# Kernel tuning notes

Hardware: AMD Instinct MI355X
Metric: run time of the kernel (lower is better)

## Reference

```python
import jax, jax.numpy as jnp
import numpy as np
import math

B, C, L, D = 64, 21, 8192, 512
KG, KP = 25, 15  # gaussian decomp kernel, phase-corrector kernel (both odd)
PI = math.pi


def _reflect_pad(x, k):
    # x: [B, C, T]; torch 'same' reflect padding: left = k//2, right = k-1-k//2
    pl = k // 2
    return jnp.pad(x, ((0, 0), (0, 0), (pl, k - 1 - pl)), mode='reflect')


def _depthwise_conv1d(x, w):
    # x: [B, C, T_pad], w: [C, 1, k]  (cross-correlation, groups=C, VALID)
    return jax.lax.conv_general_dilated(
        x, w, window_strides=(1,), padding='VALID',
        dimension_numbers=('NCH', 'OIH', 'NCH'),
        feature_group_count=x.shape[1])


def _phase_unwrap(phase):
    # phase: [B, L, C]; unwrap along time axis=1 (matches torch implementation)
    d = jnp.diff(phase, axis=1)
    d_mod = jnp.mod(d + PI, 2.0 * PI) - PI
    d_mod = jnp.where((d_mod == -PI) & (d > 0), PI, d_mod)
    correction = jnp.cumsum(d_mod - d, axis=1)
    return jnp.concatenate([phase[:, :1, :], phase[:, 1:, :] + correction], axis=1)


def _analytic_signal(x):
    # scipy.signal.hilbert along axis=1; x: [B, L, C], L even
    n = x.shape[1]
    h = np.zeros(n, dtype=np.float32)
    h[0] = 1.0
    h[n // 2] = 1.0
    h[1:n // 2] = 2.0
    Xf = jnp.fft.fft(x, axis=1)
    return jnp.fft.ifft(Xf * jnp.asarray(h)[None, :, None], axis=1)


def setup_inputs() -> dict:
    key = jax.random.key(0)
    ks = jax.random.split(key, 4)
    return {
        'x_input': jax.random.normal(ks[0], (B, C, L), jnp.float32),
        'x_w': jax.random.normal(ks[1], (L, D), jnp.float32) / np.sqrt(L).astype(np.float32),
        'x_b': jnp.zeros((D,), jnp.float32),
        'i_w': jax.random.normal(ks[2], (L, D), jnp.float32) / np.sqrt(L).astype(np.float32),
        'i_b': jnp.zeros((D,), jnp.float32),
        'log_sigma': jnp.full((C,), math.log(3.0), jnp.float32),
        'pc_weight': jax.random.normal(ks[3], (C, 1, KP), jnp.float32) * 0.01,
        'pc_strength': jnp.asarray(0.2, jnp.float32),
        'alpha_log': jnp.zeros((C,), jnp.float32),
        'phi0': jnp.zeros((C,), jnp.float32),
        'beta1_log': jnp.asarray(0.0, jnp.float32),
        'beta2_log': jnp.asarray(0.0, jnp.float32),
    }


def reference(x_input, x_w, x_b, i_w, i_b, log_sigma, pc_weight, pc_strength,
              alpha_log, phi0, beta1_log, beta2_log):
    # x_input: [B, C, L]
    x_out = jax.nn.gelu(x_input @ x_w + x_b, approximate=False)  # [B, C, D]

    # --- decomp_Gaussian (depthwise gaussian low-pass) ---
    half = KG // 2
    idx = jnp.arange(-half, half + 1, dtype=x_input.dtype)
    sigma = jnp.exp(log_sigma)[:, None, None] + 1e-6            # [C,1,1]
    g = jnp.exp(-(idx[None, None, :] ** 2) / (2.0 * sigma * sigma))
    g = g / (g.sum(axis=-1, keepdims=True) + 1e-12)             # [C,1,KG]
    trend_ch = _depthwise_conv1d(_reflect_pad(x_input, KG), g)  # [B,C,L]
    seasonal = (x_input - trend_ch).transpose(0, 2, 1)          # [B,L,C]
    trend = trend_ch.transpose(0, 2, 1)                         # [B,L,C]

    # --- TSCoupler ---
    # hilbert_transform uses .detach() in the original -> stop_gradient
    z = _analytic_signal(jax.lax.stop_gradient(seasonal))
    phase = jnp.arctan2(z.imag, z.real)                         # [B,L,C]
    phase_u = _phase_unwrap(phase)

    # ZeroMeanPhaseCorrector
    w = pc_weight - pc_weight.mean(axis=-1, keepdims=True)
    delta = _depthwise_conv1d(_reflect_pad(phase_u.transpose(0, 2, 1), KP), w)
    phi_corr = phase_u + jnp.tanh(pc_strength) * delta.transpose(0, 2, 1)
    phi_corr = phi_corr + phi0[None, None, :]

    T_clamped = jnp.clip(trend, -10.0, 10.0)
    beta1 = jax.nn.softplus(beta1_log) + 1e-6
    beta2 = jax.nn.softplus(beta2_log) + 1e-6
    A_raw = beta1 * jnp.log1p(jnp.exp(beta2 * T_clamped))       # [B,L,C]
    alpha = jax.nn.softplus(alpha_log)[None, None, :] + 1e-6    # [1,1,C]
    A_t = alpha * A_raw[0]                                      # [1,L,C]  (batch-0 indexing, as in source)
    I = (A_t * jnp.cos(phi_corr)).transpose(0, 2, 1)            # [B,C,L]

    I_coupled = jax.nn.gelu(I @ i_w + i_b, approximate=False)   # [B,C,D]
    return (x_out, I_coupled)
```

## Files before the change

### kernel.cpp

```cpp
#include <hip/hip_runtime.h>
#include <hip/hip_bf16.h>
#include <math.h>

#define LMAX 8192
#define KGAUSS 25

#define PI_F 3.14159265358979323846f
#define TWO_PI_F 6.28318530717958647692f

typedef __hip_bfloat16 bf16;
typedef unsigned short u16;
typedef short bf16x8 __attribute__((ext_vector_type(8)));
typedef float f32x4 __attribute__((ext_vector_type(4)));

__device__ __forceinline__ float b2f(bf16 v) { return __bfloat162float(v); }
__device__ __forceinline__ bf16 f2b(float v) { return __float2bfloat16(v); }
__device__ __forceinline__ float rdv(const void* p, long i, int isb) {
  return isb ? b2f(((const bf16*)p)[i]) : ((const float*)p)[i];
}

__device__ __forceinline__ void async16(const void* g, void* l) {
#if __has_builtin(__builtin_amdgcn_global_load_lds)
  __builtin_amdgcn_global_load_lds((const __attribute__((address_space(1))) void*)g,
                                   (__attribute__((address_space(3))) void*)l, 16, 0, 0);
#else
  *(uint4*)l = *(const uint4*)g;
#endif
}

__device__ __forceinline__ float2 f2add(float2 a, float2 b) {
  return make_float2(a.x + b.x, a.y + b.y);
}
__device__ __forceinline__ float2 f2sub(float2 a, float2 b) {
  return make_float2(a.x - b.x, a.y - b.y);
}
__device__ __forceinline__ float2 cmulc(float2 x, float2 w) {
  return make_float2(x.x * w.x + x.y * w.y, x.y * w.x - x.x * w.y);
}
__device__ __forceinline__ float2 cmul(float2 x, float2 w) {
  return make_float2(x.x * w.x - x.y * w.y, x.x * w.y + x.y * w.x);
}
#define ZI(i) ((i) ^ (((i) >> 4) & 15))

__global__ void k_params(const void* xb, const void* ib, const void* ls, const void* pw,
                         const void* al, const void* ph, const void* ps, const void* b1,
                         const void* b2, float* pf, int* flag, float2* tw,
                         int D, int C, int KP, int L) {
  unsigned wls = ((const unsigned*)ls)[0];
  int isb = ((wls >> 16) == (wls & 0xffffu)) ? 1 : 0;
  int blk = blockIdx.x, t = threadIdx.x;
  if (blk < 64) {
    int i = blk * 256 + t;
    if (i == 0) flag[0] = isb;
    float v = 0.0f;
    if (i < D)                              v = rdv(xb, i, isb);
    else if (i >= 2048 && i < 2048 + D)     v = rdv(ib, i - 2048, isb);
    else if (i >= 4096 && i < 4096 + C)     v = rdv(ls, i - 4096, isb);
    else if (i >= 4352 && i < 4352 + C*KP)  v = rdv(pw, i - 4352, isb);
    else if (i >= 8448 && i < 8448 + C)     v = rdv(al, i - 8448, isb);
    else if (i >= 8704 && i < 8704 + C)     v = rdv(ph, i - 8704, isb);
    else if (i == 8960)                     v = rdv(ps, 0, isb);
    else if (i == 8961)                     v = rdv(b1, 0, isb);
    else if (i == 8962)                     v = rdv(b2, 0, isb);
    pf[i] = v;
  } else {
    int j = (blk - 64) * 256 + t;
    if (j < L / 2) {
      double a = 6.283185307179586476925286766559 * (double)j / (double)L;
      tw[j] = make_float2((float)cos(a), (float)sin(a));
    }
  }
}

__global__ __launch_bounds__(256) void k_transpose(const void* __restrict__ in,
    bf16* __restrict__ out, const int* __restrict__ flag, int K, int N) {
  __shared__ u16 tile[64][65];
  int isb = *flag;
  int r0 = blockIdx.x * 64, c0 = blockIdx.y * 64;
  int t = threadIdx.x;
#pragma unroll
  for (int i = 0; i < 16; ++i) {
    int idx = t + i * 256;
    int r = idx >> 6, cc = idx & 63;
    int gr = r0 + r; gr = gr < K ? gr : K - 1;
    int gc = c0 + cc; gc = gc < N ? gc : N - 1;
    size_t gi = (size_t)gr * N + gc;
    u16 v;
    if (isb) v = ((const u16*)in)[gi];
    else { bf16 h = f2b(((const float*)in)[gi]); v = *(u16*)&h; }
    tile[r][cc] = v;
  }
  __syncthreads();
#pragma unroll
  for (int i = 0; i < 16; ++i) {
    int idx = t + i * 256;
    int a = idx >> 6, bb = idx & 63;
    if (c0 + a < N && r0 + bb < K)
      ((u16*)out)[(size_t)(c0 + a) * K + (r0 + bb)] = tile[bb][a];
  }
}

__global__ __launch_bounds__(256) void k_decomp(const void* __restrict__ x,
    const int* __restrict__ flag, const float* __restrict__ pf,
    float* __restrict__ seasonal, float* __restrict__ trend0,
    bf16* __restrict__ Xb, int C, int L) {
  __shared__ float xs[LMAX];
  int bc = blockIdx.x;
  int c = bc % C, b = bc / C;
  int t = threadIdx.x;
  int isb = *flag;
  for (int i = t; i < L; i += 256) {
    float xv = rdv(x, (size_t)bc * L + i, isb);
    xs[i] = xv;
    Xb[(size_t)bc * L + i] = f2b(xv);
  }
  float sigma = expf(pf[4096 + c]) + 1e-6f;
  float inv2s2 = 1.0f / (2.0f * sigma * sigma);
  float g[KGAUSS];
  float gs = 0.0f;
  for (int j = 0; j < KGAUSS; ++j) {
    float d = (float)(j - 12);
    float v = expf(-(d * d) * inv2s2);
    g[j] = v; gs += v;
  }
  float ginv = 1.0f / (gs + 1e-12f);
  for (int j = 0; j < KGAUSS; ++j) g[j] *= ginv;
  __syncthreads();
  for (int i = t; i < L; i += 256) {
    float acc = 0.0f;
#pragma unroll
    for (int j = 0; j < KGAUSS; ++j) {
      int idx = i + j - 12;
      idx = idx < 0 ? -idx : (idx >= L ? 2 * L - 2 - idx : idx);
      acc += g[j] * xs[idx];
    }
    seasonal[(size_t)bc * L + i] = xs[i] - acc;
    if (b == 0) trend0[(size_t)c * L + i] = acc;
  }
}

__global__ void k_amp(float* __restrict__ trend0, const float* __restrict__ pf,
                      int L) {
  int i = blockIdx.x * 256 + threadIdx.x;
  int c = blockIdx.y;
  if (i >= L) return;
  float alpha = log1pf(expf(pf[8448 + c])) + 1e-6f;
  float beta1 = log1pf(expf(pf[8961])) + 1e-6f;
  float beta2 = log1pf(expf(pf[8962])) + 1e-6f;
  size_t idx = (size_t)c * L + i;
  float T = trend0[idx];
  T = fminf(10.0f, fmaxf(-10.0f, T));
  trend0[idx] = alpha * (beta1 * log1pf(expf(beta2 * T)));
}

__global__ __launch_bounds__(512, 4) void k_hilbert8(float* __restrict__ sp,
    const float2* __restrict__ tw, int L, int lg, long M) {
  __shared__ float2 z[LMAX];
  long r0 = 2L * blockIdx.x;
  int has1 = (r0 + 1 < M) ? 1 : 0;
  float* row0 = sp + (size_t)r0 * L;
  float* row1 = row0 + (has1 ? (size_t)L : 0);
  const int t = threadIdx.x;
  const int T = 512;
  const int nq = L >> 3;

  for (int s = lg; s >= 4; s -= 3) {
    const int h4 = 1 << (s - 3);
    for (int q = t; q < nq; q += T) {
      int pos = q & (h4 - 1);
      int base = ((q >> (s - 3)) << s) + pos;
      float2 E0, E1, E2, E3, E4, E5, E6, E7;
      if (s == lg) {
        int i;
        i = base;          E0 = make_float2(row0[i], has1 ? row1[i] : 0.0f);
        i = base + h4;     E1 = make_float2(row0[i], has1 ? row1[i] : 0.0f);
        i = base + 2*h4;   E2 = make_float2(row0[i], has1 ? row1[i] : 0.0f);
        i = base + 3*h4;   E3 = make_float2(row0[i], has1 ? row1[i] : 0.0f);
        i = base + 4*h4;   E4 = make_float2(row0[i], has1 ? row1[i] : 0.0f);
        i = base + 5*h4;   E5 = make_float2(row0[i], has1 ? row1[i] : 0.0f);
        i = base + 6*h4;   E6 = make_float2(row0[i], has1 ? row1[i] : 0.0f);
        i = base + 7*h4;   E7 = make_float2(row0[i], has1 ? row1[i] : 0.0f);
      } else {
        E0 = z[ZI(base)];          E1 = z[ZI(base + h4)];
        E2 = z[ZI(base + 2*h4)];   E3 = z[ZI(base + 3*h4)];
        E4 = z[ZI(base + 4*h4)];   E5 = z[ZI(base + 5*h4)];
        E6 = z[ZI(base + 6*h4)];   E7 = z[ZI(base + 7*h4)];
      }
      float2 wa0 = tw[pos << (lg - s)];
      float2 wa1 = tw[(pos + h4) << (lg - s)];
      float2 wa2 = tw[(pos + 2*h4) << (lg - s)];
      float2 wa3 = tw[(pos + 3*h4) << (lg - s)];
      float2 wb0 = tw[pos << (lg - s + 1)];
      float2 wb1 = tw[(pos + h4) << (lg - s + 1)];
      float2 wc0 = tw[pos << (lg - s + 2)];
      float2 A0 = f2add(E0, E4), B0 = cmulc(f2sub(E0, E4), wa0);
      float2 A1 = f2add(E1, E5), B1 = cmulc(f2sub(E1, E5), wa1);
      float2 A2 = f2add(E2, E6), B2 = cmulc(f2sub(E2, E6), wa2);
      float2 A3 = f2add(E3, E7), B3 = cmulc(f2sub(E3, E7), wa3);
      float2 C0 = f2add(A0, A2), C2 = cmulc(f2sub(A0, A2), wb0);
      float2 C1 = f2add(A1, A3), C3 = cmulc(f2sub(A1, A3), wb1);
      float2 D0 = f2add(B0, B2), D2 = cmulc(f2sub(B0, B2), wb0);
      float2 D1 = f2add(B1, B3), D3 = cmulc(f2sub(B1, B3), wb1);
      z[ZI(base)]          = f2add(C0, C1);
      z[ZI(base + h4)]     = cmulc(f2sub(C0, C1), wc0);
      z[ZI(base + 2*h4)]   = f2add(C2, C3);
      z[ZI(base + 3*h4)]   = cmulc(f2sub(C2, C3), wc0);
      z[ZI(base + 4*h4)]   = f2add(D0, D1);
      z[ZI(base + 5*h4)]   = cmulc(f2sub(D0, D1), wc0);
      z[ZI(base + 6*h4)]   = f2add(D2, D3);
      z[ZI(base + 7*h4)]   = cmulc(f2sub(D2, D3), wc0);
    }
    __syncthreads();
  }
  {
    const float s1 = 1.0f / (float)L, s2 = 2.0f / (float)L;
    const int h = L >> 1;
    for (int q = t; q < (L >> 1); q += T) {
      int i0 = 2 * q, i1 = i0 + 1;
      float2 a = z[ZI(i0)], b = z[ZI(i1)];
      float2 u0 = f2add(a, b), u1 = f2sub(a, b);
      int k0 = (int)(__brev((unsigned)i0) >> (32 - lg));
      int k1 = (int)(__brev((unsigned)i1) >> (32 - lg));
      float sc0 = (k0 == 0 || k0 == h) ? s1 : (k0 < h ? s2 : 0.0f);
      float sc1 = (k1 == 0 || k1 == h) ? s1 : (k1 < h ? s2 : 0.0f);
      u0.x *= sc0; u0.y *= sc0; u1.x *= sc1; u1.y *= sc1;
      z[ZI(i0)] = f2add(u0, u1);
      z[ZI(i1)] = f2sub(u0, u1);
    }
  }
  __syncthreads();
  for (int s = 2; s + 2 <= lg; s += 3) {
    const int h = 1 << (s - 1);
    const int last = (s + 2 == lg) ? 1 : 0;
    for (int q = t; q < nq; q += T) {
      int pos = q & (h - 1);
      int base = ((q >> (s - 1)) << (s + 2)) + pos;
      float2 E0 = z[ZI(base)],         E1 = z[ZI(base + h)];
      float2 E2 = z[ZI(base + 2*h)],   E3 = z[ZI(base + 3*h)];
      float2 E4 = z[ZI(base + 4*h)],   E5 = z[ZI(base + 5*h)];
      float2 E6 = z[ZI(base + 6*h)],   E7 = z[ZI(base + 7*h)];
      float2 w0  = tw[pos << (lg - s)];
      float2 w10 = tw[pos << (lg - s - 1)];
      float2 w11 = tw[(pos + h) << (lg - s - 1)];
      float2 w20 = tw[pos << (lg - s - 2)];
      float2 w21 = tw[(pos + h) << (lg - s - 2)];
      float2 w22 = tw[(pos + 2*h) << (lg - s - 2)];
      float2 w23 = tw[(pos + 3*h) << (lg - s - 2)];
      float2 c;
      c = cmul(E1, w0); float2 A0 = f2add(E0, c), A1 = f2sub(E0, c);
      c = cmul(E3, w0); float2 A2 = f2add(E2, c), A3 = f2sub(E2, c);
      c = cmul(E5, w0); float2 A4 = f2add(E4, c), A5 = f2sub(E4, c);
      c = cmul(E7, w0); float2 A6 = f2add(E6, c), A7 = f2sub(E6, c);
      c = cmul(A2, w10); float2 B0 = f2add(A0, c), B2 = f2sub(A0, c);
      c = cmul(A3, w11); float2 B1 = f2add(A1, c), B3 = f2sub(A1, c);
      c = cmul(A6, w10); float2 B4 = f2add(A4, c), B6 = f2sub(A4, c);
      c = cmul(A7, w11); float2 B5 = f2add(A5, c), B7 = f2sub(A5, c);
      float2 F0, F1, F2, F3, F4, F5, F6, F7;
      c = cmul(B4, w20); F0 = f2add(B0, c); F4 = f2sub(B0, c);
      c = cmul(B5, w21); F1 = f2add(B1, c); F5 = f2sub(B1, c);
      c = cmul(B6, w22); F2 = f2add(B2, c); F6 = f2sub(B2, c);
      c = cmul(B7, w23); F3 = f2add(B3, c); F7 = f2sub(B3, c);
      if (last) {
        float2 ov[8] = {F0, F1, F2, F3, F4, F5, F6, F7};
#pragma unroll
        for (int j = 0; j < 8; ++j) {
          int i = base + j * h;
          float xa = row0[i];
          float xb = has1 ? row1[i] : 0.0f;
          float ha = ov[j].y - xb;
          float hb = xa - ov[j].x;
          row0[i] = atan2f(ha, xa);
          if (has1) row1[i] = atan2f(hb, xb);
        }
      } else {
        z[ZI(base)]        = F0; z[ZI(base + h)]    = F1;
        z[ZI(base + 2*h)]  = F2; z[ZI(base + 3*h)]  = F3;
        z[ZI(base + 4*h)]  = F4; z[ZI(base + 5*h)]  = F5;
        z[ZI(base + 6*h)]  = F6; z[ZI(base + 7*h)]  = F7;
      }
    }
    if (!last) __syncthreads();
  }
}

__global__ __launch_bounds__(512, 4) void k_hilbert4(float* __restrict__ sp,
    const float2* __restrict__ tw, int L, int lg, long M) {
  __shared__ float2 z[LMAX];
  long r0 = 2L * blockIdx.x;
  int has1 = (r0 + 1 < M) ? 1 : 0;
  float* row0 = sp + (size_t)r0 * L;
  float* row1 = row0 + (has1 ? (size_t)L : 0);
  const int t = threadIdx.x;
  const int T = 512;
  const int nq = L >> 2;

  {
    const int s = lg;
    const int h = 1 << (s - 1), h2 = h >> 1;
    for (int q = t; q < nq; q += T) {
      int pos = q & (h2 - 1);
      int base = ((q >> (s - 2)) << s) + pos;
      int i0 = base, i1 = base + h2, i2 = base + h, i3 = base + h + h2;
      float2 e0 = make_float2(row0[i0], has1 ? row1[i0] : 0.0f);
      float2 e1 = make_float2(row0[i1], has1 ? row1[i1] : 0.0f);
      float2 e2 = make_float2(row0[i2], has1 ? row1[i2] : 0.0f);
      float2 e3 = make_float2(row0[i3], has1 ? row1[i3] : 0.0f);
      float2 wa = tw[pos << (lg - s)];
      float2 wb = tw[(pos + h2) << (lg - s)];
      float2 wc = tw[pos << (lg - s + 1)];
      float2 t0 = f2add(e0, e2), t2 = cmulc(f2sub(e0, e2), wa);
      float2 t1 = f2add(e1, e3), t3 = cmulc(f2sub(e1, e3), wb);
      z[ZI(i0)] = f2add(t0, t1);
      z[ZI(i1)] = cmulc(f2sub(t0, t1), wc);
      z[ZI(i2)] = f2add(t2, t3);
      z[ZI(i3)] = cmulc(f2sub(t2, t3), wc);
    }
  }
  __syncthreads();
  for (int s = lg - 2; s >= 2; s -= 2) {
    const int h = 1 << (s - 1), h2 = h >> 1;
    for (int q = t; q < nq; q += T) {
      int pos = q & (h2 - 1);
      int base = ((q >> (s - 2)) << s) + pos;
      int i0 = base, i1 = base + h2, i2 = base + h, i3 = base + h + h2;
      float2 e0 = z[ZI(i0)], e1 = z[ZI(i1)], e2 = z[ZI(i2)], e3 = z[ZI(i3)];
      float2 wa = tw[pos << (lg - s)];
      float2 wb = tw[(pos + h2) << (lg - s)];
      float2 wc = tw[pos << (lg - s + 1)];
      float2 t0 = f2add(e0, e2), t2 = cmulc(f2sub(e0, e2), wa);
      float2 t1 = f2add(e1, e3), t3 = cmulc(f2sub(e1, e3), wb);
      z[ZI(i0)] = f2add(t0, t1);
      z[ZI(i1)] = cmulc(f2sub(t0, t1), wc);
      z[ZI(i2)] = f2add(t2, t3);
      z[ZI(i3)] = cmulc(f2sub(t2, t3), wc);
    }
    __syncthreads();
  }
  {
    const float s1 = 1.0f / (float)L, s2 = 2.0f / (float)L;
    const int h = L >> 1;
    if (lg & 1) {
      for (int q = t; q < (L >> 1); q += T) {
        int i0 = 2 * q, i1 = i0 + 1;
        float2 a = z[ZI(i0)], b = z[ZI(i1)];
        float2 u0 = f2add(a, b), u1 = f2sub(a, b);
        int k0 = (int)(__brev((unsigned)i0) >> (32 - lg));
        int k1 = (int)(__brev((unsigned)i1) >> (32 - lg));
        float sc0 = (k0 == 0 || k0 == h) ? s1 : (k0 < h ? s2 : 0.0f);
        float sc1 = (k1 == 0 || k1 == h) ? s1 : (k1 < h ? s2 : 0.0f);
        u0.x *= sc0; u0.y *= sc0; u1.x *= sc1; u1.y *= sc1;
        z[ZI(i0)] = f2add(u0, u1);
        z[ZI(i1)] = f2sub(u0, u1);
      }
    } else {
      for (int p = t; p < L; p += T) {
        int k = (int)(__brev((unsigned)p) >> (32 - lg));
        float sc = (k == 0 || k == h) ? s1 : (k < h ? s2 : 0.0f);
        float2 v = z[ZI(p)];
        v.x *= sc; v.y *= sc;
        z[ZI(p)] = v;
      }
    }
  }
  __syncthreads();
  const int s0 = (lg & 1) ? 2 : 1;
  for (int s = s0; s + 1 <= lg - 2; s += 2) {
    const int hs = 1 << (s - 1);
    for (int q = t; q < nq; q += T) {
      int pos = q & (hs - 1);
      int base = ((q >> (s - 1)) << (s + 1)) + pos;
      int i0 = base, i1 = base + hs, i2 = base + 2 * hs, i3 = base + 3 * hs;
      float2 e0 = z[ZI(i0)], e1 = z[ZI(i1)], e2 = z[ZI(i2)], e3 = z[ZI(i3)];
      float2 wa = tw[pos << (lg - s)];
      float2 wb = tw[pos << (lg - s - 1)];
      float2 wcc = tw[(pos + hs) << (lg - s - 1)];
      float2 c1 = cmul(e1, wa);
      float2 t0 = f2add(e0, c1), t1 = f2sub(e0, c1);
      float2 d1 = cmul(e3, wa);
      float2 t2 = f2add(e2, d1), t3 = f2sub(e2, d1);
      c1 = cmul(t2, wb);
      float2 o0 = f2add(t0, c1), o2 = f2sub(t0, c1);
      d1 = cmul(t3, wcc);
      float2 o1 = f2add(t1, d1), o3 = f2sub(t1, d1);
      z[ZI(i0)] = o0; z[ZI(i1)] = o1; z[ZI(i2)] = o2; z[ZI(i3)] = o3;
    }
    __syncthreads();
  }
  {
    const int s = lg - 1;
    const int hs = 1 << (s - 1);
    for (int q = t; q < nq; q += T) {
      int pos = q & (hs - 1);
      int base = ((q >> (s - 1)) << (s + 1)) + pos;
      int i0 = base, i1 = base + hs, i2 = base + 2 * hs, i3 = base + 3 * hs;
      float2 e0 = z[ZI(i0)], e1 = z[ZI(i1)], e2 = z[ZI(i2)], e3 = z[ZI(i3)];
      float2 wa = tw[pos << (lg - s)];
      float2 wb = tw[pos << (lg - s - 1)];
      float2 wcc = tw[(pos + hs) << (lg - s - 1)];
      float2 c1 = cmul(e1, wa);
      float2 t0 = f2add(e0, c1), t1 = f2sub(e0, c1);
      float2 d1 = cmul(e3, wa);
      float2 t2 = f2add(e2, d1), t3 = f2sub(e2, d1);
      c1 = cmul(t2, wb);
      float2 o0 = f2add(t0, c1), o2 = f2sub(t0, c1);
      d1 = cmul(t3, wcc);
      float2 o1 = f2add(t1, d1), o3 = f2sub(t1, d1);
      int idx[4] = {i0, i1, i2, i3};
      float2 ov[4] = {o0, o1, o2, o3};
#pragma unroll
      for (int j = 0; j < 4; ++j) {
        int i = idx[j];
        float xa = row0[i];
        float xb = has1 ? row1[i] : 0.0f;
        float2 w = ov[j];
        float ha = w.y - xb;
        float hb = xa - w.x;
        row0[i] = atan2f(ha, xa);
        if (has1) row1[i] = atan2f(hb, xb);
      }
    }
  }
}

__global__ __launch_bounds__(256, 4) void k_unwrap_I32(
    const float* __restrict__ phase_all, const float* __restrict__ amp,
    const float* __restrict__ pf, bf16* __restrict__ I, int C, int L) {
  __shared__ float p[LMAX + LMAX / 32];
  __shared__ int wsum[8];
  int bc = blockIdx.x, c = bc % C;
  int t = threadIdx.x;
  const float* prow = phase_all + (size_t)bc * L;
  for (int i = t; i < L; i += 256) p[i + (i >> 5)] = prow[i];
  __syncthreads();
  const int sbase = 33 * t;
  float v[32];
#pragma unroll
  for (int ii = 0; ii < 32; ++ii) v[ii] = p[sbase + ii];
  float prev = (t > 0) ? p[sbase - 2] : 0.0f;
  int run = 0;
#pragma unroll
  for (int ii = 0; ii < 32; ++ii) {
    float cur = v[ii];
    if (ii > 0 || t > 0) {
      float d = cur - prev;
      int k = (int)floorf((d + PI_F) * (1.0f / TWO_PI_F));
      float m = d - TWO_PI_F * (float)k;
      if (m == -PI_F && d > 0.0f) k -= 1;
      run -= k;
    }
    prev = cur;
    v[ii] = cur + TWO_PI_F * (float)run;
  }
  int lane = t & 63, w = t >> 6;
  int inc = run;
#pragma unroll
  for (int off = 1; off < 64; off <<= 1) {
    int n = __shfl_up(inc, off);
    if (lane >= off) inc += n;
  }
  if (lane == 63) wsum[w] = inc;
  __syncthreads();
  int base = inc - run;
  for (int ww = 0; ww < w; ++ww) base += wsum[ww];
  float fb = TWO_PI_F * (float)base;
#pragma unroll
  for (int ii = 0; ii < 32; ++ii) v[ii] += fb;
#pragma unroll
  for (int ii = 0; ii < 32; ++ii) p[sbase + ii] = v[ii];
  __syncthreads();
  float hl[7], hr[7];
#pragma unroll
  for (int m = 0; m < 7; ++m)
    hl[m] = (t == 0) ? v[7 - m] : p[sbase - 8 + m];
#pragma unroll
  for (int m = 0; m < 7; ++m)
    hr[m] = (t == 255) ? v[30 - m] : p[sbase + 33 + m];
  __syncthreads();
  float wz[15];
  float mean = 0.0f;
#pragma unroll
  for (int j = 0; j < 15; ++j) { wz[j] = pf[4352 + c * 15 + j]; mean += wz[j]; }
  mean /= 15.0f;
#pragma unroll
  for (int j = 0; j < 15; ++j) wz[j] -= mean;
  float tanh_s = tanhf(pf[8960]);
  float phi0c = pf[8704 + c];
#pragma unroll
  for (int ii = 0; ii < 32; ++ii) {
    float delta = 0.0f;
#pragma unroll
    for (int j = 0; j < 15; ++j) {
      int idx = ii + j - 7;
      float u = (idx < 0) ? hl[idx + 7] : (idx >= 32 ? hr[idx - 32] : v[idx]);
      delta = fmaf(wz[j], u, delta);
    }
    float phi = v[ii] + tanh_s * delta + phi0c;
    p[sbase + ii] = cosf(phi);
  }
  __syncthreads();
  const float* arow = amp + (size_t)c * L;
  bf16* Irow = I + (size_t)bc * L;
  for (int i = t; i < L; i += 256)
    Irow[i] = f2b(arow[i] * p[i + (i >> 5)]);
}

__global__ __launch_bounds__(256) void k_unwrap_I(const float* __restrict__ phase_all,
    const float* __restrict__ amp, const float* __restrict__ pf,
    bf16* __restrict__ I, int C, int L, int KP) {
  __shared__ float p[LMAX];
  __shared__ int ksum[256];
  int bc = blockIdx.x;
  int c = bc % C;
  int t = threadIdx.x;
  int chunk = L >> 8;
  const float* prow = phase_all + (size_t)bc * L;
  for (int i = t; i < L; i += 256) p[i] = prow[i];
  __syncthreads();
  int start = t * chunk;
  float prev0 = (t > 0) ? p[start - 1] : 0.0f;
  int kacc = 0;
  {
    float prev = prev0;
    for (int ii = 0; ii < chunk; ++ii) {
      int i = start + ii;
      float cur = p[i];
      if (i > 0) {
        float d = cur - prev;
        int k = (int)floorf((d + PI_F) * (1.0f / TWO_PI_F));
        float m = d - TWO_PI_F * (float)k;
        if (m == -PI_F && d > 0.0f) k -= 1;
        kacc -= k;
      }
      prev = cur;
    }
  }
  ksum[t] = kacc;
  __syncthreads();
  if (t == 0) {
    int run = 0;
    for (int i = 0; i < 256; ++i) { int v = ksum[i]; ksum[i] = run; run += v; }
  }
  __syncthreads();
  {
    int run = ksum[t];
    float prev = prev0;
    for (int ii = 0; ii < chunk; ++ii) {
      int i = start + ii;
      float cur = p[i];
      if (i > 0) {
        float d = cur - prev;
        int k = (int)floorf((d + PI_F) * (1.0f / TWO_PI_F));
        float m = d - TWO_PI_F * (float)k;
        if (m == -PI_F && d > 0.0f) k -= 1;
        run -= k;
      }
      prev = cur;
      p[i] = cur + TWO_PI_F * (float)run;
    }
  }
  __syncthreads();
  float wz[32];
  float mean = 0.0f;
  for (int j = 0; j < KP; ++j) { wz[j] = pf[4352 + c * KP + j]; mean += wz[j]; }
  mean /= (float)KP;
  for (int j = 0; j < KP; ++j) wz[j] -= mean;
  int hk = KP / 2;
  float tanh_s = tanhf(pf[8960]);
  float phi0c = pf[8704 + c];
  const float* arow = amp + (size_t)c * L;
  bf16* Irow = I + (size_t)bc * L;
  for (int i = t; i < L; i += 256) {
    float delta = 0.0f;
    for (int j = 0; j < KP; ++j) {
      int idx = i + j - hk;
      idx = idx < 0 ? -idx : (idx >= L ? 2 * L - 2 - idx : idx);
      delta = fmaf(wz[j], p[idx], delta);
    }
    float phi = p[i] + tanh_s * delta + phi0c;
    Irow[i] = f2b(arow[i] * cosf(phi));
  }
}

__global__ __launch_bounds__(256) void k_gemm_sk(const bf16* __restrict__ A0,
    const bf16* __restrict__ A1, const bf16* __restrict__ B0,
    const bf16* __restrict__ B1, float* __restrict__ part,
    int M, int L, int D, int KS, int KC) {
  __shared__ __align__(16) u16 As[128 * 32];
  __shared__ __align__(16) u16 Bs[128 * 32];
  int zz = blockIdx.z;
  int g = zz / KS, ks = zz - g * KS;
  const u16* Ag = (const u16*)(g ? A1 : A0);
  const u16* Bg = (const u16*)(g ? B1 : B0);
  int m0 = blockIdx.x * 128, n0 = blockIdx.y * 128;
  int t = threadIdx.x;
  int l = t & 63, w = t >> 6;
  int wm = (w >> 1) * 64, wn = (w & 1) * 64;
  int lr = l & 15, lq = l >> 4;
  f32x4 acc[4][4];
  f32x4 z4 = 0.0f;
  for (int i = 0; i < 4; ++i)
    for (int j = 0; j < 4; ++j) acc[i][j] = z4;

  int kbeg = ks * KC, kend = kbeg + KC;
  for (int k0 = kbeg; k0 < kend; k0 += 32) {
#pragma unroll
    for (int q = 0; q < 2; ++q) {
      int chunk = q * 256 + t;
      int row = chunk >> 2, kc = chunk & 3;
      int ar = m0 + row; ar = ar < M ? ar : M - 1;
      int br = n0 + row; br = br < D ? br : D - 1;
      async16(Ag + (size_t)ar * L + (k0 + kc * 8), As + chunk * 8);
      async16(Bg + (size_t)br * L + (k0 + kc * 8), Bs + chunk * 8);
    }
    __syncthreads();
    bf16x8 af[4], bfr[4];
#pragma unroll
    for (int i = 0; i < 4; ++i) {
      af[i]  = *(const bf16x8*)(As + (wm + i * 16 + lr) * 32 + lq * 8);
      bfr[i] = *(const bf16x8*)(Bs + (wn + i * 16 + lr) * 32 + lq * 8);
    }
#pragma unroll
    for (int i = 0; i < 4; ++i)
#pragma unroll
      for (int j = 0; j < 4; ++j)
        acc[i][j] = __builtin_amdgcn_mfma_f32_16x16x32_bf16(af[i], bfr[j], acc[i][j], 0, 0, 0);
    __syncthreads();
  }
  float* pbase = part + (size_t)zz * M * D;
#pragma unroll
  for (int i = 0; i < 4; ++i) {
    int rowb = m0 + wm + i * 16 + lq * 4;
#pragma unroll
    for (int j = 0; j < 4; ++j) {
      int gcol = n0 + wn + j * 16 + lr;
      if (gcol < D) {
#pragma unroll
        for (int r = 0; r < 4; ++r) {
          int grow = rowb + r;
          if (grow < M)
            pbase[(size_t)grow * D + gcol] = acc[i][j][r];
        }
      }
    }
  }
}

__global__ __launch_bounds__(256) void k_reduce(const float* __restrict__ part,
    const float* __restrict__ pf, float* __restrict__ out, long MD, int D, int KS) {
  long idx = (long)blockIdx.x * 256 + threadIdx.x;
  if (idx >= 2 * MD) return;
  int g = (int)(idx / MD);
  long r = idx - (long)g * MD;
  const float* p = part + (size_t)g * KS * MD + r;
  float s = 0.0f;
  for (int ks = 0; ks < KS; ++ks) s += p[(size_t)ks * MD];
  int d = (int)(r % (long)D);
  float v = s + pf[g * 2048 + d];
  out[idx] = 0.5f * v * (1.0f + erff(v * 0.70710678118654752f));
}

static inline int cdiv_i(long a, long b) { return (int)((a + b - 1) / b); }

extern "C" void kernel_launch(void* const* d_in, const int* in_sizes, int n_in,
                              void* d_out, int out_size, void* d_ws, size_t ws_size,
                              hipStream_t stream) {
  long B = 64, C = 21, L = 8192, D = 512, KP = 15;
  if (n_in == 12) {
    long Sx = in_sizes[0], Sw = in_sizes[1], Sb = in_sizes[2];
    long Sls = in_sizes[5], Spw = in_sizes[6];
    if (Sb > 0 && Sw % Sb == 0 && Sls > 0 && Spw % Sls == 0) {
      long Lc = Sw / Sb, KPc = Spw / Sls;
      if (Lc >= 256 && Lc <= LMAX && !(Lc & (Lc - 1)) && (KPc & 1) && KPc <= 31 &&
          Sx % (Sls * Lc) == 0) {
        L = Lc; D = Sb; C = Sls; KP = KPc; B = Sx / (Sls * Lc);
      }
    }
  }
  long M = B * C;
  int lg = 0; while ((1L << lg) < L) ++lg;

  const void* x_input = d_in[0];
  const void* x_w     = d_in[1];
  const void* x_b     = d_in[2];
  const void* i_w     = d_in[3];
  const void* i_b     = d_in[4];
  const void* lsg     = d_in[5];
  const void* pw      = d_in[6];
  const void* ps      = d_in[7];
  const void* al      = d_in[8];
  const void* ph      = d_in[9];
  const void* b1      = d_in[10];
  const void* b2      = d_in[11];

  char* ws = (char*)d_ws;
  size_t off = 0;
  auto take = [&](size_t bytes) { size_t o = off; off = (off + bytes + 255) & ~(size_t)255; return o; };
  float*  seasonal = (float*)(ws + take((size_t)M * L * 4));
  float*  trend0   = (float*)(ws + take((size_t)C * L * 4));
  bf16*   Ibuf     = (bf16*)(ws + take((size_t)M * L * 2));
  float2* tw       = (float2*)(ws + take((size_t)(L / 2) * 8));
  float*  pf       = (float*)(ws + take(65536));
  int*    flag     = (int*)(ws + take(256));
  bf16*   Xb       = (bf16*)(ws + take((size_t)M * L * 2));
  bf16*   Btx      = (bf16*)(ws + take((size_t)D * L * 2));
  bf16*   Bti      = (bf16*)(ws + take((size_t)D * L * 2));
  if (ws_size < off) return;

  int KS = 8;
  while (KS > 1 && ((L % ((long)KS * 32)) != 0 || 2L * KS * D > L)) KS >>= 1;
  float* out0 = (float*)d_out;
  float* part = (2L * KS * D <= L) ? seasonal : out0;
  int KC = (int)(L / KS);

  k_params<<<64 + cdiv_i(L / 2, 256), 256, 0, stream>>>(
      x_b, i_b, lsg, pw, al, ph, ps, b1, b2, pf, flag, tw,
      (int)D, (int)C, (int)KP, (int)L);

  k_transpose<<<dim3(cdiv_i(L, 64), cdiv_i(D, 64)), 256, 0, stream>>>(x_w, Btx, flag,
                                                                      (int)L, (int)D);
  k_transpose<<<dim3(cdiv_i(L, 64), cdiv_i(D, 64)), 256, 0, stream>>>(i_w, Bti, flag,
                                                                      (int)L, (int)D);

  k_decomp<<<(int)M, 256, 0, stream>>>(x_input, flag, pf, seasonal, trend0, Xb,
                                       (int)C, (int)L);
  k_amp<<<dim3(cdiv_i(L, 256), (int)C), 256, 0, stream>>>(trend0, pf, (int)L);
  if ((lg - 1) % 3 == 0)
    k_hilbert8<<<cdiv_i(M, 2), 512, 0, stream>>>(seasonal, tw, (int)L, lg, M);
  else
    k_hilbert4<<<cdiv_i(M, 2), 512, 0, stream>>>(seasonal, tw, (int)L, lg, M);
  if (L == 8192 && KP == 15)
    k_unwrap_I32<<<(int)M, 256, 0, stream>>>(seasonal, trend0, pf, Ibuf, (int)C, (int)L);
  else
    k_unwrap_I<<<(int)M, 256, 0, stream>>>(seasonal, trend0, pf, Ibuf, (int)C, (int)L,
                                           (int)KP);

  k_gemm_sk<<<dim3(cdiv_i(M, 128), cdiv_i(D, 128), 2 * KS), 256, 0, stream>>>(
      Xb, Ibuf, Btx, Bti, part, (int)M, (int)L, (int)D, KS, KC);
  k_reduce<<<cdiv_i(2 * M * D, 256), 256, 0, stream>>>(part, pf, out0, M * D, (int)D, KS);
}
```

Measured before the change: 401.5 us.

## Register-tile gaussian decomposition and fuse amplitude computation into decomp kernel

```diff
diff --git a/kernel.cpp b/kernel.cpp
--- a/kernel.cpp
+++ b/kernel.cpp
@@ -100,6 +100,66 @@
   }
 }
 
+__global__ __launch_bounds__(256, 4) void k_decomp32(const void* __restrict__ x,
+    const int* __restrict__ flag, const float* __restrict__ pf,
+    float* __restrict__ seasonal, float* __restrict__ trend0,
+    bf16* __restrict__ Xb, int C, int L) {
+  __shared__ float xs[LMAX + LMAX / 32];
+  int bc = blockIdx.x, c = bc % C, b = bc / C;
+  int t = threadIdx.x;
+  int isb = *flag;
+  for (int i = t; i < L; i += 256) {
+    float xv = rdv(x, (size_t)bc * L + i, isb);
+    xs[i + (i >> 5)] = xv;
+    Xb[(size_t)bc * L + i] = f2b(xv);
+  }
+  float sigma = expf(pf[4096 + c]) + 1e-6f;
+  float inv2s2 = 1.0f / (2.0f * sigma * sigma);
+  float g[KGAUSS];
+  float gs = 0.0f;
+#pragma unroll
+  for (int j = 0; j < KGAUSS; ++j) {
+    float d = (float)(j - 12);
+    float vv = expf(-(d * d) * inv2s2);
+    g[j] = vv; gs += vv;
+  }
+  float ginv = 1.0f / (gs + 1e-12f);
+#pragma unroll
+  for (int j = 0; j < KGAUSS; ++j) g[j] *= ginv;
+  __syncthreads();
+  const int base = 32 * t;
+  float v[56];
+#pragma unroll
+  for (int m = 0; m < 56; ++m) {
+    int idx = base + m - 12;
+    idx = idx < 0 ? -idx : (idx >= L ? 2 * L - 2 - idx : idx);
+    v[m] = xs[idx + (idx >> 5)];
+  }
+  __syncthreads();
+  const int sb = 33 * t;
+  float aA = 0.0f, ab1 = 0.0f, ab2 = 0.0f;
+  if (b == 0) {
+    aA  = log1pf(expf(pf[8448 + c])) + 1e-6f;
+    ab1 = log1pf(expf(pf[8961])) + 1e-6f;
+    ab2 = log1pf(expf(pf[8962])) + 1e-6f;
+  }
+  float* trow = trend0 + (size_t)c * L;
+#pragma unroll
+  for (int ii = 0; ii < 32; ++ii) {
+    float acc = 0.0f;
+#pragma unroll
+    for (int j = 0; j < KGAUSS; ++j) acc = fmaf(g[j], v[ii + j], acc);
+    xs[sb + ii] = v[ii + 12] - acc;
+    if (b == 0) {
+      float T = fminf(10.0f, fmaxf(-10.0f, acc));
+      trow[base + ii] = aA * (ab1 * log1pf(expf(ab2 * T)));
+    }
+  }
+  __syncthreads();
+  for (int i = t; i < L; i += 256)
+    seasonal[(size_t)bc * L + i] = xs[i + (i >> 5)];
+}
+
 __global__ __launch_bounds__(256) void k_decomp(const void* __restrict__ x,
     const int* __restrict__ flag, const float* __restrict__ pf,
     float* __restrict__ seasonal, float* __restrict__ trend0,
@@ -125,6 +185,9 @@
   }
   float ginv = 1.0f / (gs + 1e-12f);
   for (int j = 0; j < KGAUSS; ++j) g[j] *= ginv;
+  float aA  = log1pf(expf(pf[8448 + c])) + 1e-6f;
+  float ab1 = log1pf(expf(pf[8961])) + 1e-6f;
+  float ab2 = log1pf(expf(pf[8962])) + 1e-6f;
   __syncthreads();
   for (int i = t; i < L; i += 256) {
     float acc = 0.0f;
@@ -135,22 +198,11 @@
       acc += g[j] * xs[idx];
     }
     seasonal[(size_t)bc * L + i] = xs[i] - acc;
-    if (b == 0) trend0[(size_t)c * L + i] = acc;
-  }
-}
-
-__global__ void k_amp(float* __restrict__ trend0, const float* __restrict__ pf,
-                      int L) {
-  int i = blockIdx.x * 256 + threadIdx.x;
-  int c = blockIdx.y;
-  if (i >= L) return;
-  float alpha = log1pf(expf(pf[8448 + c])) + 1e-6f;
-  float beta1 = log1pf(expf(pf[8961])) + 1e-6f;
-  float beta2 = log1pf(expf(pf[8962])) + 1e-6f;
-  size_t idx = (size_t)c * L + i;
-  float T = trend0[idx];
-  T = fminf(10.0f, fmaxf(-10.0f, T));
-  trend0[idx] = alpha * (beta1 * log1pf(expf(beta2 * T)));
+    if (b == 0) {
+      float T = fminf(10.0f, fmaxf(-10.0f, acc));
+      trend0[(size_t)c * L + i] = aA * (ab1 * log1pf(expf(ab2 * T)));
+    }
+  }
 }
 
 __global__ __launch_bounds__(512, 4) void k_hilbert8(float* __restrict__ sp,
@@ -721,9 +773,12 @@
   k_transpose<<<dim3(cdiv_i(L, 64), cdiv_i(D, 64)), 256, 0, stream>>>(i_w, Bti, flag,
                                                                       (int)L, (int)D);
 
-  k_decomp<<<(int)M, 256, 0, stream>>>(x_input, flag, pf, seasonal, trend0, Xb,
-                                       (int)C, (int)L);
-  k_amp<<<dim3(cdiv_i(L, 256), (int)C), 256, 0, stream>>>(trend0, pf, (int)L);
+  if (L == 8192)
+    k_decomp32<<<(int)M, 256, 0, stream>>>(x_input, flag, pf, seasonal, trend0, Xb,
+                                           (int)C, (int)L);
+  else
+    k_decomp<<<(int)M, 256, 0, stream>>>(x_input, flag, pf, seasonal, trend0, Xb,
+                                         (int)C, (int)L);
   if ((lg - 1) % 3 == 0)
     k_hilbert8<<<cdiv_i(M, 2), 512, 0, stream>>>(seasonal, tw, (int)L, lg, M);
   else
```

Result: faster. 375.9 us (-6.4%).
